# Performance work log

Measured on AMD Instinct MI355X. Metric: run time of the kernel, lower is better.

## Reference

```python
import jax, jax.numpy as jnp
import numpy as np

B, S, H, V, E, C = 32, 512, 512, 32000, 768, 3
D = E + C  # LSTM input dim = embedding + one-hot prior


def setup_inputs() -> dict:
    key = jax.random.key(0)
    ks = jax.random.split(key, 13)
    p = lambda k, shape: (jax.random.normal(k, shape, jnp.float32) * 0.02)
    return {
        "embedding_table": p(ks[0], (V, E)),
        "fwd_kernel": p(ks[1], (D, 4 * H)),
        "fwd_rec_kernel": p(ks[2], (H, 4 * H)),
        "fwd_bias": p(ks[3], (4 * H,)),
        "bwd_kernel": p(ks[4], (D, 4 * H)),
        "bwd_rec_kernel": p(ks[5], (H, 4 * H)),
        "bwd_bias": p(ks[6], (4 * H,)),
        "w1": p(ks[7], (2 * H, H)),
        "b1": jnp.zeros((H,), jnp.float32),
        "w2": p(ks[8], (H, C)),
        "b2": jnp.zeros((C,), jnp.float32),
        "input_ids": jax.random.randint(ks[9], (B, S), 0, V),
        "prior_info": jax.random.randint(ks[10], (B, S), 0, C),
        "labels": jax.random.randint(ks[11], (B, S), 0, C),
    }


def _lstm(x, K, R, b, reverse):
    """Keras-style LSTM (gate order i,f,c,o). x: [B,S,D] -> [B,S,H].
    With reverse=True, lax.scan processes time backwards and emits outputs
    aligned to original positions, matching Keras Bidirectional's
    go_backwards + output re-reversal."""
    zx = jnp.einsum('bsd,dh->bsh', x, K) + b  # input projection, [B,S,4H]
    zx = jnp.swapaxes(zx, 0, 1)               # [S,B,4H]
    h0 = jnp.zeros((x.shape[0], R.shape[0]), x.dtype)

    def step(carry, z):
        h, c = carry
        z = z + h @ R
        i, f, g, o = jnp.split(z, 4, axis=-1)
        c = jax.nn.sigmoid(f) * c + jax.nn.sigmoid(i) * jnp.tanh(g)
        h = jax.nn.sigmoid(o) * jnp.tanh(c)
        return (h, c), h

    _, ys = jax.lax.scan(step, (h0, h0), zx, reverse=reverse)
    return jnp.swapaxes(ys, 0, 1)  # [B,S,H]


def reference(embedding_table, fwd_kernel, fwd_rec_kernel, fwd_bias,
              bwd_kernel, bwd_rec_kernel, bwd_bias,
              w1, b1, w2, b2, input_ids, prior_info, labels):
    emb = embedding_table[input_ids]                       # [B,S,E] gather
    prior = jax.nn.one_hot(prior_info, C, dtype=emb.dtype)  # [B,S,3]
    x = jnp.concatenate([emb, prior], axis=-1)             # [B,S,771]
    hf = _lstm(x, fwd_kernel, fwd_rec_kernel, fwd_bias, reverse=False)
    hb = _lstm(x, bwd_kernel, bwd_rec_kernel, bwd_bias, reverse=True)
    h = jnp.concatenate([hf, hb], axis=-1)                 # [B,S,2H]
    h = h @ w1 + b1                                        # Dense (linear)
    logits = h @ w2 + b2                                   # [B,S,3]
    probs = jax.nn.softmax(logits, axis=-1)
    logp = jax.nn.log_softmax(logits, axis=-1)
    lab = jax.nn.one_hot(labels, C, dtype=logp.dtype)
    loss = jnp.mean(-jnp.sum(logp * lab, axis=(-1, -2)))
    return probs, loss
```

## Files before the change

kernel.cpp:

```cpp
#include <hip/hip_runtime.h>
#include <hip/hip_bf16.h>

#define BB 32
#define SS 512
#define HH 512
#define VV 32000
#define EE 768
#define NC 3
#define G4 2048
#define MM (BB*SS)
#define SENT 0xFFFFFFFFu

typedef __attribute__((ext_vector_type(8))) short bf16x8;
typedef __attribute__((ext_vector_type(4))) float f32x4;
typedef unsigned int u32;
typedef unsigned short u16;
typedef __attribute__((ext_vector_type(4))) u32 u32x4;
typedef __attribute__((ext_vector_type(2))) u32 u32x2;

#define MFMA(a,b,c) __builtin_amdgcn_mfma_f32_16x16x32_bf16(a,b,c,0,0,0)

static __device__ __forceinline__ u16 f2bf(float f) {
  union { float f; u32 u; } v; v.f = f;
  return (u16)((v.u + 0x7fffu + ((v.u >> 16) & 1u)) >> 16);
}
static __device__ __forceinline__ float bf2f(u16 h) {
  union { u32 u; float f; } v; v.u = ((u32)h) << 16;
  return v.f;
}
static __device__ __forceinline__ float sigm(float x) { return 1.f/(1.f+__expf(-x)); }
static __device__ __forceinline__ float tanh_f(float x) {
  x = fminf(8.f, fmaxf(-8.f, x));
  float t = __expf(2.f*x);
  return (t-1.f)/(t+1.f);
}
static __device__ __forceinline__ bool ok16(u32 v) {
  return ((v & 0xFFFFu) != 0xFFFFu) && ((v >> 16) != 0xFFFFu);
}

static __device__ void conv_body(int blk, const float* __restrict__ src, u16* __restrict__ dst) {
  int i = blk * 256 + threadIdx.x;
  if (i >= VV*EE/8) return;
  const float4* s = ((const float4*)src) + (size_t)i*2;
  float4 a = s[0], b = s[1];
  u32 x = (u32)f2bf(a.x) | ((u32)f2bf(a.y) << 16);
  u32 y = (u32)f2bf(a.z) | ((u32)f2bf(a.w) << 16);
  u32 z = (u32)f2bf(b.x) | ((u32)f2bf(b.y) << 16);
  u32 w = (u32)f2bf(b.z) | ((u32)f2bf(b.w) << 16);
  ((uint4*)dst)[i] = make_uint4(x, y, z, w);
}
static __device__ void pack_body(int blk, const float* __restrict__ src, u16* __restrict__ dst, int K, int N) {
  int tid = blk * 256 + threadIdx.x;
  int nkf = K >> 5;
  int l = tid & 63, fi = tid >> 6;
  int kf = fi % nkf, nf = fi / nkf;
  if (nf >= (N >> 4)) return;
  int col = nf * 16 + (l & 15);
  int k0 = kf * 32 + (l >> 4) * 8;
  u32 o[4];
  #pragma unroll
  for (int j = 0; j < 4; ++j) {
    u16 lo = f2bf(src[(size_t)(k0 + 2*j) * N + col]);
    u16 hi = f2bf(src[(size_t)(k0 + 2*j + 1) * N + col]);
    o[j] = (u32)lo | ((u32)hi << 16);
  }
  *((uint4*)(dst + (size_t)tid * 8)) = make_uint4(o[0], o[1], o[2], o[3]);
}
__global__ __launch_bounds__(256) void k_prep(
    const float* emb, u16* embT,
    const float* fK, u16* Kfp, const float* bK, u16* Kbp,
    const float* fR, u16* Rfp, const float* bR, u16* Rbp,
    const float* w1, u16* w1p)
{
  int b = blockIdx.x;
  if      (b < 12000) conv_body(b, emb, embT);
  else if (b < 12768) pack_body(b-12000, fK, Kfp, EE, G4);
  else if (b < 13536) pack_body(b-12768, bK, Kbp, EE, G4);
  else if (b < 14048) pack_body(b-13536, fR, Rfp, HH, G4);
  else if (b < 14560) pack_body(b-14048, bR, Rbp, HH, G4);
  else                pack_body(b-14560, w1, w1p, 2*HH, HH);
}

static __device__ __forceinline__ void proj_role(
    int pid, char* smem,
    const u16* __restrict__ embT, const u16* __restrict__ Kfp, const u16* __restrict__ Kbp,
    const float* __restrict__ fb_, const float* __restrict__ bb_,
    const float* __restrict__ fK_, const float* __restrict__ bK_,
    const int* __restrict__ ids, const int* __restrict__ prior,
    u16* __restrict__ zx2f, u16* __restrict__ zx2b)
{
  int w = threadIdx.x >> 6, l = threadIdx.x & 63;
  int dir = pid >= 112;
  int i0 = dir ? pid - 112 : pid;
  const u16* Bp = dir ? Kbp : Kfp;
  const float* bias = dir ? bb_ : fb_;
  const float* Kp = (dir ? bK_ : fK_) + (size_t)EE * G4;
  u16* zx2 = dir ? zx2b : zx2f;
  u16* lt = (u16*)smem;
  for (int i = i0; i < 2048; i += 112) {
    int mtseq = i >> 4, nt = i & 15;
    int mt = dir ? (127 - mtseq) : mtseq;
    int m0 = mt * 128 + w * 32;
    int r0 = m0 + (l & 15);
    int id0 = ids[(r0 & 31) * SS + (r0 >> 5)];
    int id1 = ids[((r0 + 16) & 31) * SS + ((r0 + 16) >> 5)];
    const u16* a0p = embT + (size_t)id0 * EE + (l >> 4) * 8;
    const u16* a1p = embT + (size_t)id1 * EE + (l >> 4) * 8;
    f32x4 acc[2][8];
    #pragma unroll
    for (int a = 0; a < 2; ++a)
      #pragma unroll
      for (int j = 0; j < 8; ++j) acc[a][j] = (f32x4){0.f,0.f,0.f,0.f};
    const u16* bbase = Bp + ((size_t)(nt*8)*24)*512 + (size_t)l*8;
    for (int kf = 0; kf < 24; ++kf) {
      bf16x8 a0 = *(const bf16x8*)(a0p + kf*32);
      bf16x8 a1 = *(const bf16x8*)(a1p + kf*32);
      #pragma unroll
      for (int nf = 0; nf < 8; ++nf) {
        bf16x8 bv = *(const bf16x8*)(bbase + (size_t)(nf*24 + kf)*512);
        acc[0][nf] = MFMA(a0, bv, acc[0][nf]);
        acc[1][nf] = MFMA(a1, bv, acc[1][nf]);
      }
    }
    __syncthreads();
    #pragma unroll
    for (int mi = 0; mi < 2; ++mi) {
      #pragma unroll
      for (int r = 0; r < 4; ++r) {
        int rloc = w*32 + mi*16 + (l >> 4)*4 + r;
        int row = mt*128 + rloc;
        int p = prior[(row & 31) * SS + (row >> 5)];
        const float* kr = Kp + (size_t)p * G4;
        #pragma unroll
        for (int nf = 0; nf < 8; ++nf) {
          int lc = (l & 15) + nf*16;
          int colg = nt*128 + lc;
          lt[rloc*136 + lc] = f2bf(acc[mi][nf][r] + bias[colg] + kr[colg]);
        }
      }
    }
    __syncthreads();
    int g = nt >> 2, cqb = (nt & 3) * 32;
    int cql = threadIdx.x & 31;
    #pragma unroll
    for (int k = 0; k < 8; ++k) {
      int rloc = k*16 + (threadIdx.x >> 5);
      int s = mt*4 + (rloc >> 5);
      int b = rloc & 31;
      u32x2 v0 = *(const u32x2*)(lt + rloc*136 + cql*4);
      u32x2 v1 = *(const u32x2*)(lt + (rloc+8)*136 + cql*4);
      u16* d0 = zx2 + (((size_t)(s*BB + b)*128 + cqb + cql)*16 + g*4);
      int rloc1 = rloc + 8;
      int s1 = mt*4 + (rloc1 >> 5), b1 = rloc1 & 31;
      u16* d1 = zx2 + (((size_t)(s1*BB + b1)*128 + cqb + cql)*16 + g*4);
      asm volatile("global_store_dwordx2 %0, %1, off sc0 sc1" :: "v"(d0), "v"(v0) : "memory");
      asm volatile("global_store_dwordx2 %0, %1, off sc0 sc1" :: "v"(d1), "v"(v1) : "memory");
    }
  }
}

__global__ __launch_bounds__(256, 1) void k_fused(
    const u16* __restrict__ embT, const u16* __restrict__ Kfp, const u16* __restrict__ Kbp,
    const float* __restrict__ fb, const float* __restrict__ bb,
    const float* __restrict__ fK, const float* __restrict__ bK,
    const int* __restrict__ ids, const int* __restrict__ prior,
    u16* __restrict__ zx2f, u16* __restrict__ zx2b,
    const u16* __restrict__ Rf, const u16* __restrict__ Rb,
    u16* __restrict__ hf, u16* __restrict__ hb)
{
  __shared__ char smem[50176];
  char* hstage = smem;
  float (*zbuf)[32][33] = (float (*)[32][33])(smem + 33280);

  int wg = blockIdx.x;
  if (wg >= 32) {
    proj_role(wg - 32, smem, embT, Kfp, Kbp, fb, bb, fK, bK, ids, prior, zx2f, zx2b);
    return;
  }
  int dir = wg >> 4, wgi = wg & 15;
  const u16* zx2 = dir ? zx2b : zx2f;
  const u16* Rp = dir ? Rb : Rf;
  u16* hbuf = dir ? hb : hf;
  int tid = threadIdx.x;
  int g = tid >> 6, l = tid & 63;
  int ncb0 = g*32 + wgi*2;
  bf16x8 rb0[16], rb1[16];
  #pragma unroll
  for (int kf = 0; kf < 16; ++kf) {
    rb0[kf] = *(const bf16x8*)(Rp + (((size_t)ncb0*16 + kf)*64 + l)*8);
    rb1[kf] = *(const bf16x8*)(Rp + (((size_t)(ncb0+1)*16 + kf)*64 + l)*8);
  }

  int eb = tid >> 3;
  int q = tid & 7;
  int colq = wgi*8 + q;
  const char* sread0 = hstage + (l & 15)*1040 + (l >> 4)*16;
  const char* sread1 = sread0 + 16*1040;
  char* swrite = hstage + (tid >> 3)*1040 + q*16;
  size_t goff = (size_t)(tid >> 3)*1024 + q*16;

  float c0 = 0.f, c1 = 0.f, c2 = 0.f, c3 = 0.f;
  for (int step = 0; step < SS; ++step) {
    int t = dir ? (SS - 1 - step) : step;
    const char* zxp = (const char*)(zx2 + ((size_t)(t*BB + eb)*128 + colq)*16);
    u32x4 ZA, ZB;
    #define LDZ() do { \
      asm volatile("global_load_dwordx4 %0, %1, off sc0 sc1" : "=v"(ZA) : "v"(zxp) : "memory"); \
      asm volatile("global_load_dwordx4 %0, %1, off offset:16 sc0 sc1" : "=v"(ZB) : "v"(zxp) : "memory"); \
    } while(0)
    #define ZOK (ok16(ZA[0]) && ok16(ZA[1]) && ok16(ZA[2]) && ok16(ZA[3]) \
              && ok16(ZB[0]) && ok16(ZB[1]) && ok16(ZB[2]) && ok16(ZB[3]))
    f32x4 a00 = {0.f,0.f,0.f,0.f}, a01 = {0.f,0.f,0.f,0.f};
    f32x4 a10 = {0.f,0.f,0.f,0.f}, a11 = {0.f,0.f,0.f,0.f};
    if (step > 0) {
      int tp = dir ? t + 1 : t - 1;
      const char* gsrc = (const char*)(hbuf + (size_t)tp*BB*HH) + goff;
      u32x4 S0, S1, S2, S3, S4, S5, S6, S7;
      #define LDC(r, off) asm volatile("global_load_dwordx4 %0, %1, off " off " sc0 sc1" \
                                       : "=v"(r) : "v"(gsrc) : "memory")
      for (;;) {
        LDZ();
        LDC(S0, "");            LDC(S1, "offset:128");
        LDC(S2, "offset:256");  LDC(S3, "offset:384");
        LDC(S4, "offset:512");  LDC(S5, "offset:640");
        LDC(S6, "offset:768");  LDC(S7, "offset:896");
        asm volatile("s_waitcnt vmcnt(0)" ::: "memory");
        __builtin_amdgcn_sched_barrier(0);
        bool ok = ZOK
               && S0[0]!=SENT && S0[1]!=SENT && S0[2]!=SENT && S0[3]!=SENT
               && S1[0]!=SENT && S1[1]!=SENT && S1[2]!=SENT && S1[3]!=SENT
               && S2[0]!=SENT && S2[1]!=SENT && S2[2]!=SENT && S2[3]!=SENT
               && S3[0]!=SENT && S3[1]!=SENT && S3[2]!=SENT && S3[3]!=SENT
               && S4[0]!=SENT && S4[1]!=SENT && S4[2]!=SENT && S4[3]!=SENT
               && S5[0]!=SENT && S5[1]!=SENT && S5[2]!=SENT && S5[3]!=SENT
               && S6[0]!=SENT && S6[1]!=SENT && S6[2]!=SENT && S6[3]!=SENT
               && S7[0]!=SENT && S7[1]!=SENT && S7[2]!=SENT && S7[3]!=SENT;
        if (__all(ok)) break;
        __builtin_amdgcn_s_sleep(1);
      }
      #undef LDC
      __builtin_amdgcn_sched_barrier(0);
      *(u32x4*)(swrite)       = S0;
      *(u32x4*)(swrite + 128) = S1;
      *(u32x4*)(swrite + 256) = S2;
      *(u32x4*)(swrite + 384) = S3;
      *(u32x4*)(swrite + 512) = S4;
      *(u32x4*)(swrite + 640) = S5;
      *(u32x4*)(swrite + 768) = S6;
      *(u32x4*)(swrite + 896) = S7;
      __syncthreads();
      #pragma unroll
      for (int kf = 0; kf < 16; ++kf) {
        bf16x8 f0 = *(const bf16x8*)(sread0 + kf*64);
        bf16x8 f1 = *(const bf16x8*)(sread1 + kf*64);
        a00 = MFMA(f0, rb0[kf], a00);
        a01 = MFMA(f0, rb1[kf], a01);
        a10 = MFMA(f1, rb0[kf], a10);
        a11 = MFMA(f1, rb1[kf], a11);
      }
    } else {
      for (;;) {
        LDZ();
        asm volatile("s_waitcnt vmcnt(0)" ::: "memory");
        __builtin_amdgcn_sched_barrier(0);
        if (__all(ZOK)) break;
        __builtin_amdgcn_s_sleep(1);
      }
      __builtin_amdgcn_sched_barrier(0);
    }
    #undef LDZ
    #undef ZOK
    int zc = l & 15;
    int zr = (l >> 4) * 4;
    #pragma unroll
    for (int r = 0; r < 4; ++r) {
      zbuf[g][zc][zr + r]           = a00[r];
      zbuf[g][16 + zc][zr + r]      = a01[r];
      zbuf[g][zc][16 + zr + r]      = a10[r];
      zbuf[g][16 + zc][16 + zr + r] = a11[r];
    }
    __syncthreads();
    int ecb = q * 4;
    float z0[4], z1[4], z2[4], z3[4];
    #pragma unroll
    for (int j = 0; j < 4; ++j) {
      z0[j] = zbuf[0][ecb + j][eb];
      z1[j] = zbuf[1][ecb + j][eb];
      z2[j] = zbuf[2][ecb + j][eb];
      z3[j] = zbuf[3][ecb + j][eb];
    }
    z0[0] += bf2f((u16)(ZA[0] & 0xffffu)); z0[1] += bf2f((u16)(ZA[0] >> 16));
    z0[2] += bf2f((u16)(ZA[1] & 0xffffu)); z0[3] += bf2f((u16)(ZA[1] >> 16));
    z1[0] += bf2f((u16)(ZA[2] & 0xffffu)); z1[1] += bf2f((u16)(ZA[2] >> 16));
    z1[2] += bf2f((u16)(ZA[3] & 0xffffu)); z1[3] += bf2f((u16)(ZA[3] >> 16));
    z2[0] += bf2f((u16)(ZB[0] & 0xffffu)); z2[1] += bf2f((u16)(ZB[0] >> 16));
    z2[2] += bf2f((u16)(ZB[1] & 0xffffu)); z2[3] += bf2f((u16)(ZB[1] >> 16));
    z3[0] += bf2f((u16)(ZB[2] & 0xffffu)); z3[1] += bf2f((u16)(ZB[2] >> 16));
    z3[2] += bf2f((u16)(ZB[3] & 0xffffu)); z3[3] += bf2f((u16)(ZB[3] >> 16));
    c0 = sigm(z1[0])*c0 + sigm(z0[0])*tanh_f(z2[0]);
    c1 = sigm(z1[1])*c1 + sigm(z0[1])*tanh_f(z2[1]);
    c2 = sigm(z1[2])*c2 + sigm(z0[2])*tanh_f(z2[2]);
    c3 = sigm(z1[3])*c3 + sigm(z0[3])*tanh_f(z2[3]);
    float h0 = sigm(z3[0])*tanh_f(c0);
    float h1 = sigm(z3[1])*tanh_f(c1);
    float h2 = sigm(z3[2])*tanh_f(c2);
    float h3 = sigm(z3[3])*tanh_f(c3);
    u32x2 hpk;
    hpk[0] = (u32)f2bf(h0) | ((u32)f2bf(h1) << 16);
    hpk[1] = (u32)f2bf(h2) | ((u32)f2bf(h3) << 16);
    u16* hp = hbuf + ((size_t)t*BB + eb)*HH + wgi*32 + q*4;
    asm volatile("global_store_dwordx2 %0, %1, off sc0 sc1" :: "v"(hp), "v"(hpk) : "memory");
  }
}

__global__ __launch_bounds__(256) void k_dense(
    const u16* __restrict__ hf, const u16* __restrict__ hb,
    const u16* __restrict__ w1p, const float* __restrict__ b1,
    u16* __restrict__ h1)
{
  int mt = blockIdx.x, nt = blockIdx.y;
  int w = threadIdx.x >> 6, l = threadIdx.x & 63;
  int m0 = mt*128 + w*32;
  int r0 = m0 + (l & 15);
  const u16* f0 = hf + (size_t)r0*HH + (l >> 4)*8;
  const u16* f1 = hf + (size_t)(r0+16)*HH + (l >> 4)*8;
  const u16* g0 = hb + (size_t)r0*HH + (l >> 4)*8;
  const u16* g1 = hb + (size_t)(r0+16)*HH + (l >> 4)*8;
  f32x4 acc[2][8];
  #pragma unroll
  for (int i = 0; i < 2; ++i)
    #pragma unroll
    for (int j = 0; j < 8; ++j) acc[i][j] = (f32x4){0.f,0.f,0.f,0.f};
  const u16* bbase = w1p + ((size_t)(nt*8)*32)*512 + (size_t)l*8;
  for (int kf = 0; kf < 32; ++kf) {
    const u16* s0 = (kf < 16) ? (f0 + kf*32) : (g0 + (kf-16)*32);
    const u16* s1 = (kf < 16) ? (f1 + kf*32) : (g1 + (kf-16)*32);
    bf16x8 a0 = *(const bf16x8*)s0;
    bf16x8 a1 = *(const bf16x8*)s1;
    #pragma unroll
    for (int nf = 0; nf < 8; ++nf) {
      bf16x8 bv = *(const bf16x8*)(bbase + (size_t)(nf*32 + kf)*512);
      acc[0][nf] = MFMA(a0, bv, acc[0][nf]);
      acc[1][nf] = MFMA(a1, bv, acc[1][nf]);
    }
  }
  int cb = nt*128 + (l & 15);
  #pragma unroll
  for (int mi = 0; mi < 2; ++mi) {
    #pragma unroll
    for (int r = 0; r < 4; ++r) {
      int row = m0 + mi*16 + (l >> 4)*4 + r;
      #pragma unroll
      for (int nf = 0; nf < 8; ++nf) {
        int col = cb + nf*16;
        h1[(size_t)row*HH + col] = f2bf(acc[mi][nf][r] + b1[col]);
      }
    }
  }
}

__global__ __launch_bounds__(256) void k_out(
    const u16* __restrict__ h1, const float* __restrict__ w2, const float* __restrict__ b2,
    const int* __restrict__ labels, float* __restrict__ out, float* __restrict__ part)
{
  int w = threadIdx.x >> 6, l = threadIdx.x & 63;
  float w2r[8][3];
  #pragma unroll
  for (int i = 0; i < 8; ++i)
    #pragma unroll
    for (int c = 0; c < 3; ++c) w2r[i][c] = w2[(l*8 + i)*3 + c];
  float b20 = b2[0], b21 = b2[1], b22 = b2[2];
  float nll = 0.f;
  int base = (blockIdx.x*4 + w)*16;
  for (int r = 0; r < 16; ++r) {
    int row = base + r;
    bf16x8 hv = *(const bf16x8*)(h1 + (size_t)row*HH + l*8);
    float s0 = 0.f, s1 = 0.f, s2 = 0.f;
    #pragma unroll
    for (int i = 0; i < 8; ++i) {
      float x = bf2f((u16)hv[i]);
      s0 += x*w2r[i][0]; s1 += x*w2r[i][1]; s2 += x*w2r[i][2];
    }
    #pragma unroll
    for (int off = 32; off > 0; off >>= 1) {
      s0 += __shfl_down(s0, off);
      s1 += __shfl_down(s1, off);
      s2 += __shfl_down(s2, off);
    }
    if (l == 0) {
      float l0 = s0+b20, l1 = s1+b21, l2 = s2+b22;
      float m = fmaxf(l0, fmaxf(l1, l2));
      float e0 = __expf(l0-m), e1 = __expf(l1-m), e2 = __expf(l2-m);
      float Z = e0+e1+e2, inv = 1.f/Z;
      int b = row & 31, s = row >> 5;
      float* po = out + ((size_t)b*SS + s)*3;
      po[0] = e0*inv; po[1] = e1*inv; po[2] = e2*inv;
      int lab = labels[b*SS + s];
      float ll = (lab == 0) ? l0 : (lab == 1 ? l1 : l2);
      nll += (m + __logf(Z)) - ll;
    }
  }
  __shared__ float ps[4];
  if (l == 0) ps[w] = nll;
  __syncthreads();
  if (threadIdx.x == 0) part[blockIdx.x] = ps[0]+ps[1]+ps[2]+ps[3];
}

__global__ void k_loss(const float* __restrict__ part, float* __restrict__ out) {
  __shared__ float sh[256];
  sh[threadIdx.x] = part[threadIdx.x];
  __syncthreads();
  for (int s = 128; s > 0; s >>= 1) {
    if (threadIdx.x < s) sh[threadIdx.x] += sh[threadIdx.x + s];
    __syncthreads();
  }
  if (threadIdx.x == 0) out[(size_t)MM*NC] = sh[0] / (float)BB;
}

extern "C" void kernel_launch(void* const* d_in, const int* in_sizes, int n_in,
                              void* d_out, int out_size, void* d_ws, size_t ws_size,
                              hipStream_t stream) {
  (void)in_sizes; (void)n_in; (void)out_size;
  const float* emb = (const float*)d_in[0];
  const float* fK  = (const float*)d_in[1];
  const float* fR  = (const float*)d_in[2];
  const float* fb  = (const float*)d_in[3];
  const float* bK  = (const float*)d_in[4];
  const float* bR  = (const float*)d_in[5];
  const float* bb  = (const float*)d_in[6];
  const float* w1  = (const float*)d_in[7];
  const float* b1  = (const float*)d_in[8];
  const float* w2  = (const float*)d_in[9];
  const float* b2  = (const float*)d_in[10];
  const int* ids   = (const int*)d_in[11];
  const int* prior = (const int*)d_in[12];
  const int* labels= (const int*)d_in[13];

  size_t off = 0;
  auto take = [&](size_t bytes) -> char* {
    char* p = (char*)d_ws + off;
    off += (bytes + 255) & ~(size_t)255;
    return p;
  };
  u16* embT = (u16*)take((size_t)VV*EE*2);
  u16* Kfp  = (u16*)take((size_t)EE*G4*2);
  u16* Kbp  = (u16*)take((size_t)EE*G4*2);
  u16* Rfp  = (u16*)take((size_t)HH*G4*2);
  u16* Rbp  = (u16*)take((size_t)HH*G4*2);
  u16* w1p  = (u16*)take((size_t)(2*HH)*HH*2);
  u16* zxf  = (u16*)take((size_t)MM*G4*2);
  u16* zxb  = (u16*)take((size_t)MM*G4*2);
  u16* hf   = (u16*)take((size_t)MM*HH*2);
  u16* hb   = (u16*)take((size_t)MM*HH*2);
  u16* h1   = (u16*)take((size_t)MM*HH*2);
  float* part = (float*)take(256*4);
  if (off > ws_size) return;

  hipMemsetAsync(zxf, 0xFF, (size_t)MM*G4*2, stream);
  hipMemsetAsync(zxb, 0xFF, (size_t)MM*G4*2, stream);
  hipMemsetAsync(hf, 0xFF, (size_t)MM*HH*2, stream);
  hipMemsetAsync(hb, 0xFF, (size_t)MM*HH*2, stream);
  k_prep<<<14816, 256, 0, stream>>>(emb, embT, fK, Kfp, bK, Kbp, fR, Rfp, bR, Rbp, w1, w1p);
  k_fused<<<256, 256, 0, stream>>>(embT, Kfp, Kbp, fb, bb, fK, bK, ids, prior,
                                   zxf, zxb, Rfp, Rbp, hf, hb);
  k_dense<<<dim3(128,4), 256, 0, stream>>>(hf, hb, w1p, b1, h1);
  k_out<<<256, 256, 0, stream>>>(h1, w2, b2, labels, (float*)d_out, part);
  k_loss<<<1, 256, 0, stream>>>(part, (float*)d_out);
}
```

Baseline: 2.250 ms.

## Collapse linear dense layers into one matrix and fuse head into persistent kernel

Because the two dense layers have no activation between them, w1 and w2 are pre-multiplied into a single 1024x3 matrix plus a combined bias in the prep kernel. This removes the large 16384x1024x512 dense GEMM and the h1 intermediate buffer. The output head (logits, softmax, NLL partials) now runs inside the fused kernel on the projection blocks once their projection work is done. Those blocks poll the hf/hb sentinel values, so the head overlaps the LSTM recurrence and two kernel launches go away. LSTM h stores are also staged through LDS and written as coalesced 16-byte stores. The cost is extra spin-polling traffic on the recurrence outputs and slightly different float rounding from the collapsed weights.

```diff
diff --git a/kernel.cpp b/kernel.cpp
--- a/kernel.cpp
+++ b/kernel.cpp
@@ -66,11 +66,28 @@
   }
   *((uint4*)(dst + (size_t)tid * 8)) = make_uint4(o[0], o[1], o[2], o[3]);
 }
+static __device__ void collapse_body(int blk, const float* __restrict__ w1,
+    const float* __restrict__ w2, const float* __restrict__ b1, const float* __restrict__ b2,
+    float* __restrict__ Wc, float* __restrict__ Wb) {
+  int g = blk * 256 + threadIdx.x;
+  if (g < 3072) {
+    int r = g / 3, c = g % 3;
+    float acc = 0.f;
+    for (int k = 0; k < HH; ++k) acc += w1[(size_t)r*HH + k] * w2[k*3 + c];
+    Wc[g] = acc;
+  } else if (g < 3075) {
+    int c = g - 3072;
+    float acc = b2[c];
+    for (int k = 0; k < HH; ++k) acc += b1[k] * w2[k*3 + c];
+    Wb[c] = acc;
+  }
+}
 __global__ __launch_bounds__(256) void k_prep(
     const float* emb, u16* embT,
     const float* fK, u16* Kfp, const float* bK, u16* Kbp,
     const float* fR, u16* Rfp, const float* bR, u16* Rbp,
-    const float* w1, u16* w1p)
+    const float* w1, const float* w2, const float* b1, const float* b2,
+    float* Wc, float* Wb)
 {
   int b = blockIdx.x;
   if      (b < 12000) conv_body(b, emb, embT);
@@ -78,7 +95,7 @@
   else if (b < 13536) pack_body(b-12768, bK, Kbp, EE, G4);
   else if (b < 14048) pack_body(b-13536, fR, Rfp, HH, G4);
   else if (b < 14560) pack_body(b-14048, bR, Rbp, HH, G4);
-  else                pack_body(b-14560, w1, w1p, 2*HH, HH);
+  else                collapse_body(b-14560, w1, w2, b1, b2, Wc, Wb);
 }
 
 static __device__ __forceinline__ void proj_role(
@@ -159,6 +176,83 @@
   }
 }
 
+static __device__ __forceinline__ void out_role(
+    int p, char* smem, const float* __restrict__ Wc, const float* __restrict__ Wb,
+    const u16* __restrict__ hf, const u16* __restrict__ hb,
+    const int* __restrict__ labels, float* __restrict__ out, float* __restrict__ part)
+{
+  if (p >= 128) return;
+  int k = p >> 1;
+  int j = (p & 1) ? (64 + k) : (63 - k);
+  __syncthreads();
+  float* Wl = (float*)smem;
+  for (int i = threadIdx.x; i < 3072; i += 256) Wl[i] = Wc[i];
+  __syncthreads();
+  float wb0 = Wb[0], wb1 = Wb[1], wb2 = Wb[2];
+  int wv = threadIdx.x >> 6, l = threadIdx.x & 63;
+  int s = j*4 + wv;
+  float nll = 0.f;
+  for (int b4 = 0; b4 < 32; b4 += 4) {
+    const char* fbase = (const char*)(hf + ((size_t)s*BB + b4)*HH) + l*16;
+    const char* gbase = (const char*)(hb + ((size_t)s*BB + b4)*HH) + l*16;
+    union { u32x4 u; u16 h[8]; } F[4], G[4];
+    for (;;) {
+      #define LDH(r) do { \
+        asm volatile("global_load_dwordx4 %0, %1, off offset:%2 sc0 sc1" \
+                     : "=v"(F[r].u) : "v"(fbase), "i"(r*1024) : "memory"); \
+        asm volatile("global_load_dwordx4 %0, %1, off offset:%2 sc0 sc1" \
+                     : "=v"(G[r].u) : "v"(gbase), "i"(r*1024) : "memory"); \
+      } while(0)
+      LDH(0); LDH(1); LDH(2); LDH(3);
+      #undef LDH
+      asm volatile("s_waitcnt vmcnt(0)" ::: "memory");
+      __builtin_amdgcn_sched_barrier(0);
+      bool ok = true;
+      #pragma unroll
+      for (int r = 0; r < 4; ++r) {
+        #pragma unroll
+        for (int d = 0; d < 4; ++d)
+          ok = ok && ok16(F[r].u[d]) && ok16(G[r].u[d]);
+      }
+      if (__all(ok)) break;
+      __builtin_amdgcn_s_sleep(64);
+    }
+    __builtin_amdgcn_sched_barrier(0);
+    #pragma unroll
+    for (int r = 0; r < 4; ++r) {
+      int b = b4 + r;
+      float s0 = 0.f, s1 = 0.f, s2 = 0.f;
+      #pragma unroll
+      for (int i = 0; i < 8; ++i) {
+        float xf = bf2f(F[r].h[i]);
+        const float* wr = Wl + (l*8 + i)*3;
+        s0 += xf*wr[0]; s1 += xf*wr[1]; s2 += xf*wr[2];
+        float xg = bf2f(G[r].h[i]);
+        const float* wr2 = Wl + (512 + l*8 + i)*3;
+        s0 += xg*wr2[0]; s1 += xg*wr2[1]; s2 += xg*wr2[2];
+      }
+      #pragma unroll
+      for (int off = 32; off > 0; off >>= 1) {
+        s0 += __shfl_down(s0, off);
+        s1 += __shfl_down(s1, off);
+        s2 += __shfl_down(s2, off);
+      }
+      if (l == 0) {
+        float l0 = s0+wb0, l1 = s1+wb1, l2 = s2+wb2;
+        float m = fmaxf(l0, fmaxf(l1, l2));
+        float e0 = __expf(l0-m), e1 = __expf(l1-m), e2 = __expf(l2-m);
+        float Z = e0+e1+e2, inv = 1.f/Z;
+        float* po = out + ((size_t)b*SS + s)*3;
+        po[0] = e0*inv; po[1] = e1*inv; po[2] = e2*inv;
+        int lab = labels[b*SS + s];
+        float ll = (lab == 0) ? l0 : (lab == 1 ? l1 : l2);
+        nll += (m + __logf(Z)) - ll;
+      }
+    }
+  }
+  if (l == 0) part[j*4 + wv] = nll;
+}
+
 __global__ __launch_bounds__(256, 1) void k_fused(
     const u16* __restrict__ embT, const u16* __restrict__ Kfp, const u16* __restrict__ Kbp,
     const float* __restrict__ fb, const float* __restrict__ bb,
@@ -166,15 +260,19 @@
     const int* __restrict__ ids, const int* __restrict__ prior,
     u16* __restrict__ zx2f, u16* __restrict__ zx2b,
     const u16* __restrict__ Rf, const u16* __restrict__ Rb,
-    u16* __restrict__ hf, u16* __restrict__ hb)
+    u16* __restrict__ hf, u16* __restrict__ hb,
+    const float* __restrict__ Wc, const float* __restrict__ Wb,
+    const int* __restrict__ labels, float* __restrict__ out, float* __restrict__ part)
 {
-  __shared__ char smem[50176];
+  __shared__ char smem[52224];
   char* hstage = smem;
   float (*zbuf)[32][33] = (float (*)[32][33])(smem + 33280);
+  char* hcoal = smem + 50176;
 
   int wg = blockIdx.x;
   if (wg >= 32) {
     proj_role(wg - 32, smem, embT, Kfp, Kbp, fb, bb, fK, bK, ids, prior, zx2f, zx2b);
+    out_role(wg - 32, smem, Wc, Wb, hf, hb, labels, out, part);
     return;
   }
   int dir = wg >> 4, wgi = wg & 15;
@@ -283,11 +381,11 @@
     int ecb = q * 4;
     float z0[4], z1[4], z2[4], z3[4];
     #pragma unroll
-    for (int j = 0; j < 4; ++j) {
-      z0[j] = zbuf[0][ecb + j][eb];
-      z1[j] = zbuf[1][ecb + j][eb];
-      z2[j] = zbuf[2][ecb + j][eb];
-      z3[j] = zbuf[3][ecb + j][eb];
+    for (int jx = 0; jx < 4; ++jx) {
+      z0[jx] = zbuf[0][ecb + jx][eb];
+      z1[jx] = zbuf[1][ecb + jx][eb];
+      z2[jx] = zbuf[2][ecb + jx][eb];
+      z3[jx] = zbuf[3][ecb + jx][eb];
     }
     z0[0] += bf2f((u16)(ZA[0] & 0xffffu)); z0[1] += bf2f((u16)(ZA[0] >> 16));
     z0[2] += bf2f((u16)(ZA[1] & 0xffffu)); z0[3] += bf2f((u16)(ZA[1] >> 16));
@@ -308,107 +406,20 @@
     u32x2 hpk;
     hpk[0] = (u32)f2bf(h0) | ((u32)f2bf(h1) << 16);
     hpk[1] = (u32)f2bf(h2) | ((u32)f2bf(h3) << 16);
-    u16* hp = hbuf + ((size_t)t*BB + eb)*HH + wgi*32 + q*4;
-    asm volatile("global_store_dwordx2 %0, %1, off sc0 sc1" :: "v"(hp), "v"(hpk) : "memory");
-  }
-}
-
-__global__ __launch_bounds__(256) void k_dense(
-    const u16* __restrict__ hf, const u16* __restrict__ hb,
-    const u16* __restrict__ w1p, const float* __restrict__ b1,
-    u16* __restrict__ h1)
-{
-  int mt = blockIdx.x, nt = blockIdx.y;
-  int w = threadIdx.x >> 6, l = threadIdx.x & 63;
-  int m0 = mt*128 + w*32;
-  int r0 = m0 + (l & 15);
-  const u16* f0 = hf + (size_t)r0*HH + (l >> 4)*8;
-  const u16* f1 = hf + (size_t)(r0+16)*HH + (l >> 4)*8;
-  const u16* g0 = hb + (size_t)r0*HH + (l >> 4)*8;
-  const u16* g1 = hb + (size_t)(r0+16)*HH + (l >> 4)*8;
-  f32x4 acc[2][8];
-  #pragma unroll
-  for (int i = 0; i < 2; ++i)
-    #pragma unroll
-    for (int j = 0; j < 8; ++j) acc[i][j] = (f32x4){0.f,0.f,0.f,0.f};
-  const u16* bbase = w1p + ((size_t)(nt*8)*32)*512 + (size_t)l*8;
-  for (int kf = 0; kf < 32; ++kf) {
-    const u16* s0 = (kf < 16) ? (f0 + kf*32) : (g0 + (kf-16)*32);
-    const u16* s1 = (kf < 16) ? (f1 + kf*32) : (g1 + (kf-16)*32);
-    bf16x8 a0 = *(const bf16x8*)s0;
-    bf16x8 a1 = *(const bf16x8*)s1;
-    #pragma unroll
-    for (int nf = 0; nf < 8; ++nf) {
-      bf16x8 bv = *(const bf16x8*)(bbase + (size_t)(nf*32 + kf)*512);
-      acc[0][nf] = MFMA(a0, bv, acc[0][nf]);
-      acc[1][nf] = MFMA(a1, bv, acc[1][nf]);
-    }
-  }
-  int cb = nt*128 + (l & 15);
-  #pragma unroll
-  for (int mi = 0; mi < 2; ++mi) {
-    #pragma unroll
-    for (int r = 0; r < 4; ++r) {
-      int row = m0 + mi*16 + (l >> 4)*4 + r;
-      #pragma unroll
-      for (int nf = 0; nf < 8; ++nf) {
-        int col = cb + nf*16;
-        h1[(size_t)row*HH + col] = f2bf(acc[mi][nf][r] + b1[col]);
-      }
-    }
-  }
-}
-
-__global__ __launch_bounds__(256) void k_out(
-    const u16* __restrict__ h1, const float* __restrict__ w2, const float* __restrict__ b2,
-    const int* __restrict__ labels, float* __restrict__ out, float* __restrict__ part)
-{
-  int w = threadIdx.x >> 6, l = threadIdx.x & 63;
-  float w2r[8][3];
-  #pragma unroll
-  for (int i = 0; i < 8; ++i)
-    #pragma unroll
-    for (int c = 0; c < 3; ++c) w2r[i][c] = w2[(l*8 + i)*3 + c];
-  float b20 = b2[0], b21 = b2[1], b22 = b2[2];
-  float nll = 0.f;
-  int base = (blockIdx.x*4 + w)*16;
-  for (int r = 0; r < 16; ++r) {
-    int row = base + r;
-    bf16x8 hv = *(const bf16x8*)(h1 + (size_t)row*HH + l*8);
-    float s0 = 0.f, s1 = 0.f, s2 = 0.f;
-    #pragma unroll
-    for (int i = 0; i < 8; ++i) {
-      float x = bf2f((u16)hv[i]);
-      s0 += x*w2r[i][0]; s1 += x*w2r[i][1]; s2 += x*w2r[i][2];
-    }
-    #pragma unroll
-    for (int off = 32; off > 0; off >>= 1) {
-      s0 += __shfl_down(s0, off);
-      s1 += __shfl_down(s1, off);
-      s2 += __shfl_down(s2, off);
-    }
-    if (l == 0) {
-      float l0 = s0+b20, l1 = s1+b21, l2 = s2+b22;
-      float m = fmaxf(l0, fmaxf(l1, l2));
-      float e0 = __expf(l0-m), e1 = __expf(l1-m), e2 = __expf(l2-m);
-      float Z = e0+e1+e2, inv = 1.f/Z;
-      int b = row & 31, s = row >> 5;
-      float* po = out + ((size_t)b*SS + s)*3;
-      po[0] = e0*inv; po[1] = e1*inv; po[2] = e2*inv;
-      int lab = labels[b*SS + s];
-      float ll = (lab == 0) ? l0 : (lab == 1 ? l1 : l2);
-      nll += (m + __logf(Z)) - ll;
-    }
-  }
-  __shared__ float ps[4];
-  if (l == 0) ps[w] = nll;
-  __syncthreads();
-  if (threadIdx.x == 0) part[blockIdx.x] = ps[0]+ps[1]+ps[2]+ps[3];
+    *(u32x2*)(hcoal + eb*64 + q*8) = hpk;
+    __syncthreads();
+    if (tid < 128) {
+      int b = tid >> 2, ch = tid & 3;
+      u32x4 v = *(const u32x4*)(hcoal + b*64 + ch*16);
+      char* hp = (char*)(hbuf + ((size_t)t*BB + b)*HH + wgi*32) + ch*16;
+      asm volatile("global_store_dwordx4 %0, %1, off sc0 sc1" :: "v"(hp), "v"(v) : "memory");
+    }
+  }
 }
 
 __global__ void k_loss(const float* __restrict__ part, float* __restrict__ out) {
   __shared__ float sh[256];
-  sh[threadIdx.x] = part[threadIdx.x];
+  sh[threadIdx.x] = part[threadIdx.x] + part[threadIdx.x + 256];
   __syncthreads();
   for (int s = 128; s > 0; s >>= 1) {
     if (threadIdx.x < s) sh[threadIdx.x] += sh[threadIdx.x + s];
@@ -447,23 +458,23 @@
   u16* Kbp  = (u16*)take((size_t)EE*G4*2);
   u16* Rfp  = (u16*)take((size_t)HH*G4*2);
   u16* Rbp  = (u16*)take((size_t)HH*G4*2);
-  u16* w1p  = (u16*)take((size_t)(2*HH)*HH*2);
   u16* zxf  = (u16*)take((size_t)MM*G4*2);
   u16* zxb  = (u16*)take((size_t)MM*G4*2);
   u16* hf   = (u16*)take((size_t)MM*HH*2);
   u16* hb   = (u16*)take((size_t)MM*HH*2);
-  u16* h1   = (u16*)take((size_t)MM*HH*2);
-  float* part = (float*)take(256*4);
+  float* Wc = (float*)take(3072*4);
+  float* Wb = (float*)take(16);
+  float* part = (float*)take(512*4);
   if (off > ws_size) return;
 
   hipMemsetAsync(zxf, 0xFF, (size_t)MM*G4*2, stream);
   hipMemsetAsync(zxb, 0xFF, (size_t)MM*G4*2, stream);
   hipMemsetAsync(hf, 0xFF, (size_t)MM*HH*2, stream);
   hipMemsetAsync(hb, 0xFF, (size_t)MM*HH*2, stream);
-  k_prep<<<14816, 256, 0, stream>>>(emb, embT, fK, Kfp, bK, Kbp, fR, Rfp, bR, Rbp, w1, w1p);
+  k_prep<<<14573, 256, 0, stream>>>(emb, embT, fK, Kfp, bK, Kbp, fR, Rfp, bR, Rbp,
+                                    w1, w2, b1, b2, Wc, Wb);
   k_fused<<<256, 256, 0, stream>>>(embT, Kfp, Kbp, fb, bb, fK, bK, ids, prior,
-                                   zxf, zxb, Rfp, Rbp, hf, hb);
-  k_dense<<<dim3(128,4), 256, 0, stream>>>(hf, hb, w1p, b1, h1);
-  k_out<<<256, 256, 0, stream>>>(h1, w2, b2, labels, (float*)d_out, part);
+                                   zxf, zxb, Rfp, Rbp, hf, hb,
+                                   Wc, Wb, labels, (float*)d_out, part);
   k_loss<<<1, 256, 0, stream>>>(part, (float*)d_out);
 }
```

Result: no change. 2.218 ms (-1.5%).
